# Kernel tuning notes

Measured on AMD Instinct MI355X. Metric: run time of the kernel, lower is better.

## Reference

```python
import jax, jax.numpy as jnp
import numpy as np

EPS = 1e-5
N_GROUPS = 32
N_HEAD = 1


def group_norm(x, gamma, beta):
    B, C, H, W = x.shape
    xg = x.reshape(B, N_GROUPS, C // N_GROUPS, H, W)
    mean = xg.mean(axis=(2, 3, 4), keepdims=True)
    var = xg.var(axis=(2, 3, 4), keepdims=True)
    xg = (xg - mean) * jax.lax.rsqrt(var + EPS)
    x = xg.reshape(B, C, H, W)
    return x * gamma[None, :, None, None] + beta[None, :, None, None]


def setup_inputs() -> dict:
    key = jax.random.key(0)
    k1, k2, k3 = jax.random.split(key, 3)
    B, C, H, W = 32, 512, 32, 32
    x = jax.random.normal(k1, (B, C, H, W), dtype=jnp.float32)
    gamma = jnp.ones((C,), dtype=jnp.float32)
    beta = jnp.zeros((C,), dtype=jnp.float32)
    # fan_avg uniform init for 1x1 convs (bound = sqrt(3*scale/fan_avg))
    bound_qkv = np.sqrt(3.0 / ((C + 3 * C) / 2))
    w_qkv = jax.random.uniform(k2, (3 * C, C), dtype=jnp.float32,
                               minval=-bound_qkv, maxval=bound_qkv)
    b_qkv = jnp.zeros((3 * C,), dtype=jnp.float32)
    bound_out = np.sqrt(3.0 * 1e-10 / C)
    w_out = jax.random.uniform(k3, (C, C), dtype=jnp.float32,
                               minval=-bound_out, maxval=bound_out)
    b_out = jnp.zeros((C,), dtype=jnp.float32)
    return {"x": x, "gamma": gamma, "beta": beta,
            "w_qkv": w_qkv, "b_qkv": b_qkv, "w_out": w_out, "b_out": b_out}


def reference(x, gamma, beta, w_qkv, b_qkv, w_out, b_out):
    B, C, H, W = x.shape
    n_head = N_HEAD
    head_dim = C // n_head
    norm = group_norm(x, gamma, beta)
    # 1x1 conv == channel matmul: [B,3C,H,W]
    qkv = jnp.einsum('bchw,oc->bohw', norm, w_qkv) + b_qkv[None, :, None, None]
    qkv = qkv.reshape(B, n_head, 3 * head_dim, H, W)
    q, k, v = jnp.split(qkv, 3, axis=2)  # each [B,n,hd,H,W]
    scale = 1.0 / np.sqrt(head_dim)
    attn = jnp.einsum('bnchw,bncyx->bnhwyx', q, k) * scale
    attn = jax.nn.softmax(attn.reshape(B, n_head, H, W, H * W), axis=-1)
    attn = attn.reshape(B, n_head, H, W, H, W)
    out = jnp.einsum('bnhwyx,bncyx->bnchw', attn, v).reshape(B, C, H, W)
    out = jnp.einsum('bchw,oc->bohw', out, w_out) + b_out[None, :, None, None]
    return out + x
```

## Files before the change

### kernel.cpp

```cpp
#include <hip/hip_runtime.h>
#include <hip/hip_bf16.h>

#define B_    32
#define C_    512
#define S_    1024
#define G_    32
#define CPG_  16
#define EPS_  1e-5f
#define SCALE_ 0.044194173824159216f
#define ZS_    1024.0f
#define VS_    1048576.0f
#define INVZS_ 0.0009765625f
#define INVVS_ 9.5367431640625e-07f

typedef __attribute__((ext_vector_type(4))) float  floatx4;
typedef __attribute__((ext_vector_type(8))) __bf16 bf16x8;
typedef long lng;

__device__ __forceinline__ float bf2f(unsigned short u) {
    union { unsigned int i; float f; } v; v.i = ((unsigned int)u) << 16; return v.f;
}
__device__ __forceinline__ unsigned short f2bf(float f) {
    union { float f; unsigned int i; } v; v.f = f;
    unsigned int r = v.i + 0x7fffu + ((v.i >> 16) & 1u);
    return (unsigned short)(r >> 16);
}
__device__ __forceinline__ unsigned int f2f8x4(float a, float b, float c, float d) {
    unsigned int v = (unsigned int)__builtin_amdgcn_cvt_pk_fp8_f32(a, b, 0, false);
    v = (unsigned int)__builtin_amdgcn_cvt_pk_fp8_f32(c, d, (int)v, true);
    return v;
}

__device__ __forceinline__ void gl16(const void* g, void* l) {
    __builtin_amdgcn_global_load_lds(
        (const __attribute__((address_space(1))) unsigned int*)g,
        (__attribute__((address_space(3))) unsigned int*)l, 16, 0, 0);
}

__global__ __launch_bounds__(256) void gnxnt(const float* __restrict__ x,
                                             const float* __restrict__ gamma,
                                             const float* __restrict__ beta,
                                             unsigned char* __restrict__ xnt,
                                             float* __restrict__ lbuf) {
    const int bid = blockIdx.x;
    const int b = bid >> 5, g = bid & 31;
    if (threadIdx.x < 8)
        ((float4*)lbuf)[bid * 8 + threadIdx.x] = make_float4(0.f, 0.f, 0.f, 0.f);

    __shared__ float tile[16 * 1025];
    __shared__ float a1[4], a2[4];
    const float* xb = x + (size_t)b * (C_ * S_) + (size_t)g * (CPG_ * S_);
    const int t = threadIdx.x;

    float s = 0.f, ss = 0.f;
    #pragma unroll
    for (int k = 0; k < 16; k++) {
        int idx = t + k * 256;
        float4 v = ((const float4*)xb)[idx];
        int c = idx >> 8, s4 = (idx & 255) * 4;
        float* dst = tile + c * 1025 + s4;
        dst[0] = v.x; dst[1] = v.y; dst[2] = v.z; dst[3] = v.w;
        s  += v.x + v.y + v.z + v.w;
        ss += v.x * v.x + v.y * v.y + v.z * v.z + v.w * v.w;
    }
    #pragma unroll
    for (int o = 32; o; o >>= 1) { s += __shfl_down(s, o); ss += __shfl_down(ss, o); }
    const int wid = t >> 6, lane = t & 63;
    if (lane == 0) { a1[wid] = s; a2[wid] = ss; }
    __syncthreads();
    float S  = a1[0] + a1[1] + a1[2] + a1[3];
    float SS = a2[0] + a2[1] + a2[2] + a2[3];
    float mean = S * (1.f / 16384.f);
    float var  = SS * (1.f / 16384.f) - mean * mean;
    float rstd = rsqrtf(var + EPS_);

    const int c0 = g * 16, cc = (t & 3) * 4;
    float av[4], bv[4];
    #pragma unroll
    for (int i = 0; i < 4; i++) {
        float a_ = rstd * gamma[c0 + cc + i];
        av[i] = a_; bv[i] = beta[c0 + cc + i] - mean * a_;
    }
    unsigned char* xo = xnt + (size_t)b * (S_ * C_) + c0 + cc;
    #pragma unroll
    for (int p = 0; p < 16; p++) {
        int srow = p * 64 + (t >> 2);
        const float* col = tile + srow;
        unsigned int o4 = f2f8x4(av[0] * col[(cc + 0) * 1025] + bv[0],
                                 av[1] * col[(cc + 1) * 1025] + bv[1],
                                 av[2] * col[(cc + 2) * 1025] + bv[2],
                                 av[3] * col[(cc + 3) * 1025] + bv[3]);
        *(unsigned int*)(xo + (size_t)srow * C_) = o4;
    }
}

__global__ __launch_bounds__(256) void tcast(const float* __restrict__ w,
                                             const float* __restrict__ w_out,
                                             unsigned short* __restrict__ WqT,
                                             unsigned short* __restrict__ WkT,
                                             unsigned short* __restrict__ WvT,
                                             unsigned short* __restrict__ Woutb) {
    const int z = blockIdx.z;
    const int m0 = blockIdx.y * 64, c0 = blockIdx.x * 64;
    const int t = threadIdx.x, tr = t >> 4, tc4 = (t & 15) * 4;
    if (z == 3) {
        #pragma unroll
        for (int i = 0; i < 4; i++) {
            int r = tr + i * 16;
            float4 v = *(const float4*)(w_out + (size_t)(m0 + r) * 512 + c0 + tc4);
            ushort4 o4;
            o4.x = f2bf(v.x); o4.y = f2bf(v.y); o4.z = f2bf(v.z); o4.w = f2bf(v.w);
            *(ushort4*)(Woutb + (size_t)(m0 + r) * 512 + c0 + tc4) = o4;
        }
        return;
    }
    const float* src = w + (size_t)z * 262144;
    unsigned short* dst = (z == 0) ? WqT : (z == 1) ? WkT : WvT;
    __shared__ float tile[64][65];
    #pragma unroll
    for (int i = 0; i < 4; i++) {
        int r = tr + i * 16;
        float4 v = *(const float4*)(src + (size_t)(m0 + r) * 512 + c0 + tc4);
        tile[r][tc4 + 0] = v.x; tile[r][tc4 + 1] = v.y;
        tile[r][tc4 + 2] = v.z; tile[r][tc4 + 3] = v.w;
    }
    __syncthreads();
    #pragma unroll
    for (int i = 0; i < 4; i++) {
        int sr = tr + i * 16;
        ushort4 o4;
        o4.x = f2bf(tile[tc4 + 0][sr]); o4.y = f2bf(tile[tc4 + 1][sr]);
        o4.z = f2bf(tile[tc4 + 2][sr]); o4.w = f2bf(tile[tc4 + 3][sr]);
        *(ushort4*)(dst + (size_t)(c0 + sr) * 512 + m0 + tc4) = o4;
    }
}

__global__ __launch_bounds__(256) void vecprep(const unsigned short* __restrict__ WkT,
                                               const float* __restrict__ w_out,
                                               const float* __restrict__ b_qkv,
                                               float* __restrict__ bzv) {
    const int o = blockIdx.x, t = threadIdx.x;
    float us = 0.f, bv = 0.f;
    #pragma unroll
    for (int mm = 0; mm < 2; mm++) {
        int m = t + mm * 256;
        us += b_qkv[m] * bf2f(WkT[(size_t)o * 512 + m]);
        bv += w_out[(size_t)o * 512 + m] * b_qkv[1024 + m];
    }
    #pragma unroll
    for (int sh = 32; sh; sh >>= 1) { us += __shfl_down(us, sh); bv += __shfl_down(bv, sh); }
    __shared__ float a[2][4];
    const int wid = t >> 6, lane = t & 63;
    if (lane == 0) { a[0][wid] = us; a[1][wid] = bv; }
    __syncthreads();
    if (t == 0) {
        bzv[o]       = (a[0][0] + a[0][1] + a[0][2] + a[0][3]) * SCALE_ * ZS_;
        bzv[512 + o] = (a[1][0] + a[1][1] + a[1][2] + a[1][3]) * VS_;
    }
}

template<bool SWAP>
__device__ __forceinline__ void mfma_loop(const unsigned short* __restrict__ Ag, int lda,
                                          const unsigned short* __restrict__ Bg, int ldb,
                                          int K, int m0, int n0,
                                          unsigned short* ldsA, unsigned short* ldsB,
                                          floatx4 (&acc)[4][4]) {
    const int t = threadIdx.x, lane = t & 63, wave = t >> 6;
    const int wr = (wave >> 1) * 64, wc = (wave & 1) * 64;
    const int lrow = lane & 15, lq = lane >> 4;
    const int srow = wave * 16 + (lane >> 2);
    const int scol = (lane & 3) * 8;
    const unsigned short* gA0 = Ag + (size_t)(m0 + srow) * lda + scol;
    const unsigned short* gA1 = gA0 + (size_t)64 * lda;
    const unsigned short* gB0 = Bg + (size_t)(n0 + srow) * ldb + scol;
    const unsigned short* gB1 = gB0 + (size_t)64 * ldb;
    unsigned short* lA = ldsA + wave * 512;
    unsigned short* lB = ldsB + wave * 512;
    for (int k0 = 0; k0 < K; k0 += 64) {
        gl16(gA0 + k0,      lA);
        gl16(gA1 + k0,      lA + 2048);
        gl16(gA0 + k0 + 32, lA + 4096);
        gl16(gA1 + k0 + 32, lA + 6144);
        gl16(gB0 + k0,      lB);
        gl16(gB1 + k0,      lB + 2048);
        gl16(gB0 + k0 + 32, lB + 4096);
        gl16(gB1 + k0 + 32, lB + 6144);
        __syncthreads();
        #pragma unroll
        for (int sub = 0; sub < 2; sub++) {
            bf16x8 af[4], bfr[4];
            #pragma unroll
            for (int i = 0; i < 4; i++) {
                af[i]  = *(const bf16x8*)(ldsA + sub * 4096 + (wr + i * 16 + lrow) * 32 + lq * 8);
                bfr[i] = *(const bf16x8*)(ldsB + sub * 4096 + (wc + i * 16 + lrow) * 32 + lq * 8);
            }
            #pragma unroll
            for (int i = 0; i < 4; i++)
                #pragma unroll
                for (int j = 0; j < 4; j++) {
                    if (SWAP)
                        acc[i][j] = __builtin_amdgcn_mfma_f32_16x16x32_bf16(bfr[j], af[i], acc[i][j], 0, 0, 0);
                    else
                        acc[i][j] = __builtin_amdgcn_mfma_f32_16x16x32_bf16(af[i], bfr[j], acc[i][j], 0, 0, 0);
                }
        }
        __syncthreads();
    }
}

__global__ __launch_bounds__(256) void prep_gemm(const unsigned short* __restrict__ WkT,
                                                 const unsigned short* __restrict__ WqT,
                                                 const unsigned short* __restrict__ Woutb,
                                                 const unsigned short* __restrict__ WvT,
                                                 unsigned char* __restrict__ Wzv) {
    __shared__ __align__(16) unsigned short ldsA[2 * 128 * 32];
    __shared__ __align__(16) unsigned short ldsB[2 * 128 * 32];
    const int z = blockIdx.z;
    const int m0 = blockIdx.y * 128, n0 = blockIdx.x * 128;
    const int t = threadIdx.x, lane = t & 63, wave = t >> 6;
    const int wr = (wave >> 1) * 64, wc = (wave & 1) * 64;
    const int lrow = lane & 15, lq = lane >> 4;
    floatx4 acc[4][4];
    #pragma unroll
    for (int i = 0; i < 4; i++)
        #pragma unroll
        for (int j = 0; j < 4; j++) acc[i][j] = (floatx4){0.f, 0.f, 0.f, 0.f};
    const unsigned short* Ag = z ? Woutb : WkT;
    const unsigned short* Bg = z ? WvT   : WqT;
    mfma_loop<true>(Ag, 512, Bg, 512, 512, m0, n0, ldsA, ldsB, acc);
    const float sc = z ? VS_ : (SCALE_ * ZS_);
    #pragma unroll
    for (int i = 0; i < 4; i++)
        #pragma unroll
        for (int j = 0; j < 4; j++) {
            int row = z * 512 + m0 + wr + i * 16 + lrow;
            int col = n0 + wc + j * 16 + lq * 4;
            floatx4 v = acc[i][j];
            unsigned int o4 = f2f8x4(v[0] * sc, v[1] * sc, v[2] * sc, v[3] * sc);
            *(unsigned int*)(Wzv + (size_t)row * 512 + col) = o4;
        }
}

template<bool SWAP>
__device__ __forceinline__ void mfma256f8_loop(const unsigned char* __restrict__ Ag, int lda,
                                               const unsigned char* __restrict__ Bg, int ldb,
                                               int nt, int m0, int n0,
                                               unsigned char* lds, floatx4 (&acc)[8][4]) {
    const int tid  = threadIdx.x;
    const int lane = tid & 63, wave = tid >> 6;
    const int wm = wave >> 2, wn = wave & 3;
    const int lrow = lane & 15, lq = lane >> 4;
    const int swz  = (lrow >> 1) & 3;
    const int hb   = (lq & 1) * 8;
    const int slb  = lq >> 1;
    const int s0 = ((slb    ) ^ swz) * 16 + hb;
    const int s1 = ((slb + 2) ^ swz) * 16 + hb;

    int aof[8], bof[4];
    #pragma unroll
    for (int i = 0; i < 8; i++) aof[i] = (wm * 128 + i * 16 + lrow) * 64;
    #pragma unroll
    for (int j = 0; j < 4; j++) bof[j] = 65536 + (wn * 64 + j * 16 + lrow) * 64;

    const int sr  = tid >> 2;
    const int scs = (tid & 3) ^ ((tid >> 3) & 3);
    const unsigned char* gA = Ag + (size_t)(m0 + sr) * lda + scs * 16;
    const unsigned char* gB = Bg + (size_t)(n0 + sr) * ldb + scs * 16;
    const size_t a128 = (size_t)128 * lda, b128 = (size_t)128 * ldb;
    unsigned char* lwA = lds + wave * 1024;
    unsigned char* lwB = lds + 65536 + wave * 1024;

#define STAGE_A(t, kh) do { \
    unsigned char* lb_ = lwA + ((t) & 1) * 32768 + (kh) * 16384; \
    const unsigned char* gp_ = gA + (t) * 128 + (kh) * 64; \
    gl16(gp_, lb_); gl16(gp_ + a128, lb_ + 8192); } while (0)
#define STAGE_B(t, kh) do { \
    unsigned char* lb_ = lwB + ((t) & 1) * 32768 + (kh) * 16384; \
    const unsigned char* gp_ = gB + (t) * 128 + (kh) * 64; \
    gl16(gp_, lb_); gl16(gp_ + b128, lb_ + 8192); } while (0)

    STAGE_A(0, 0); STAGE_B(0, 0); STAGE_A(0, 1); STAGE_B(0, 1);
    asm volatile("s_waitcnt vmcnt(4)" ::: "memory");
    __builtin_amdgcn_s_barrier();

    lng af0[8], af1[8], bf0[4], bf1[4];
    for (int u = 0; u < nt; ++u) {
        const int p = u & 1;
        #pragma unroll
        for (int kh = 0; kh < 2; ++kh) {
            const int slab = p * 32768 + kh * 16384;
            #pragma unroll
            for (int j = 0; j < 4; j++) {
                bf0[j] = *(const lng*)(lds + slab + bof[j] + s0);
                bf1[j] = *(const lng*)(lds + slab + bof[j] + s1);
            }
            #pragma unroll
            for (int i = 0; i < 8; i++) {
                af0[i] = *(const lng*)(lds + slab + aof[i] + s0);
                af1[i] = *(const lng*)(lds + slab + aof[i] + s1);
            }
            if (u + 1 < nt) { STAGE_A(u + 1, kh); STAGE_B(u + 1, kh); }
            __builtin_amdgcn_s_barrier();
            asm volatile("s_waitcnt lgkmcnt(0)" ::: "memory");
            __builtin_amdgcn_sched_barrier(0);
            __builtin_amdgcn_s_setprio(1);
            #pragma unroll
            for (int i = 0; i < 8; i++)
                #pragma unroll
                for (int j = 0; j < 4; j++) {
                    if (SWAP)
                        acc[i][j] = __builtin_amdgcn_mfma_f32_16x16x32_fp8_fp8(
                            bf0[j], af0[i], acc[i][j], 0, 0, 0);
                    else
                        acc[i][j] = __builtin_amdgcn_mfma_f32_16x16x32_fp8_fp8(
                            af0[i], bf0[j], acc[i][j], 0, 0, 0);
                }
            #pragma unroll
            for (int i = 0; i < 8; i++)
                #pragma unroll
                for (int j = 0; j < 4; j++) {
                    if (SWAP)
                        acc[i][j] = __builtin_amdgcn_mfma_f32_16x16x32_fp8_fp8(
                            bf1[j], af1[i], acc[i][j], 0, 0, 0);
                    else
                        acc[i][j] = __builtin_amdgcn_mfma_f32_16x16x32_fp8_fp8(
                            af1[i], bf1[j], acc[i][j], 0, 0, 0);
                }
            __builtin_amdgcn_s_setprio(0);
            if (u < nt - 1) {
                asm volatile("s_waitcnt vmcnt(4)" ::: "memory");
                __builtin_amdgcn_s_barrier();
            } else if (kh == 0) {
                asm volatile("s_waitcnt vmcnt(0)" ::: "memory");
                __builtin_amdgcn_s_barrier();
            }
        }
    }
#undef STAGE_A
#undef STAGE_B
}

#define GEMMF8_VARS                                                   \
    __shared__ __align__(16) unsigned char lds[131072];               \
    const int lane = threadIdx.x & 63, wave = threadIdx.x >> 6;       \
    const int wm = wave >> 2, wn = wave & 3;                          \
    const int lrow = lane & 15, lq = lane >> 4;                       \
    floatx4 acc[8][4];                                                \
    _Pragma("unroll") for (int i = 0; i < 8; i++)                     \
        _Pragma("unroll") for (int j = 0; j < 4; j++)                 \
            acc[i][j] = (floatx4){0.f, 0.f, 0.f, 0.f};

__global__ __launch_bounds__(512, 2) void zv_mfma(const unsigned char* __restrict__ Wzv,
                                                  const unsigned char* __restrict__ xnt,
                                                  const float* __restrict__ bzv,
                                                  unsigned char* __restrict__ Zb,
                                                  unsigned char* __restrict__ Vb) {
    const int f = blockIdx.x;
    const int xcd = f & 7, j = f >> 3;
    const int b = xcd + 8 * (j >> 4);
    const int tile = j & 15;
    const int m0 = (tile >> 2) * 256, n0 = (tile & 3) * 256;
    GEMMF8_VARS
    const unsigned char* Bg = xnt + (size_t)b * (S_ * C_);
    if (m0 < 512) {
        mfma256f8_loop<false>(Wzv, C_, Bg, C_, 4, m0, n0, lds, acc);
        unsigned char* dst = Zb + (size_t)b * (S_ * C_);
        #pragma unroll
        for (int i = 0; i < 8; i++)
            #pragma unroll
            for (int j2 = 0; j2 < 4; j2++) {
                int oabs = m0 + wm * 128 + i * 16 + lq * 4;
                int s    = n0 + wn * 64 + j2 * 16 + lrow;
                float4 bi = *(const float4*)(bzv + oabs);
                floatx4 v = acc[i][j2];
                unsigned int o4 = f2f8x4(v[0] + bi.x, v[1] + bi.y,
                                         v[2] + bi.z, v[3] + bi.w);
                *(unsigned int*)(dst + (size_t)s * C_ + oabs) = o4;
            }
    } else {
        mfma256f8_loop<true>(Wzv, C_, Bg, C_, 4, m0, n0, lds, acc);
        unsigned char* dst = Vb + (size_t)b * (C_ * S_);
        #pragma unroll
        for (int i = 0; i < 8; i++)
            #pragma unroll
            for (int j2 = 0; j2 < 4; j2++) {
                int row = m0 + wm * 128 + i * 16 + lrow;
                int c   = row - 512;
                int sb  = n0 + wn * 64 + j2 * 16 + lq * 4;
                float bi = bzv[row];
                floatx4 v = acc[i][j2];
                unsigned int o4 = f2f8x4(v[0] + bi, v[1] + bi, v[2] + bi, v[3] + bi);
                *(unsigned int*)(dst + (size_t)c * S_ + sb) = o4;
            }
    }
}

__global__ __launch_bounds__(512, 2) void scores_exp(const unsigned char* __restrict__ Zb,
                                                     const unsigned char* __restrict__ xnt,
                                                     unsigned char* __restrict__ Pb,
                                                     float* __restrict__ l) {
    const int f = blockIdx.x;
    const int xcd = f & 7, j = f >> 3;
    const int b = xcd + 8 * (j >> 4);
    const int tile = j & 15;
    const int m0 = (tile >> 2) * 256, n0 = (tile & 3) * 256;
    GEMMF8_VARS
    const unsigned char* Ag = Zb  + (size_t)b * (S_ * C_);
    const unsigned char* Bg = xnt + (size_t)b * (S_ * C_);
    mfma256f8_loop<true>(Ag, C_, Bg, C_, 4, m0, n0, lds, acc);
    unsigned char* pp = Pb + (size_t)b * ((size_t)S_ * S_);
    float* lb = l + b * S_;
    float rsv[8];
    #pragma unroll
    for (int i = 0; i < 8; i++) {
        int q = m0 + wm * 128 + i * 16 + lrow;
        float rs = 0.f;
        #pragma unroll
        for (int j2 = 0; j2 < 4; j2++) {
            int kv = n0 + wn * 64 + j2 * 16 + lq * 4;
            floatx4 v = acc[i][j2];
            float e0 = __expf(v[0] * INVZS_), e1 = __expf(v[1] * INVZS_);
            float e2 = __expf(v[2] * INVZS_), e3 = __expf(v[3] * INVZS_);
            rs += (e0 + e1) + (e2 + e3);
            *(unsigned int*)(pp + (size_t)q * S_ + kv) = f2f8x4(e0, e1, e2, e3);
        }
        rs += __shfl_xor(rs, 16);
        rs += __shfl_xor(rs, 32);
        rsv[i] = rs;
    }
    __syncthreads();
    float* sred = (float*)lds;
    if (lane < 16) {
        #pragma unroll
        for (int i = 0; i < 8; i++)
            sred[wn * 256 + wm * 128 + i * 16 + lrow] = rsv[i];
    }
    __syncthreads();
    if (threadIdx.x < 256) {
        int q = threadIdx.x;
        float sum = (sred[q] + sred[256 + q]) + (sred[512 + q] + sred[768 + q]);
        atomicAdd(lb + m0 + q, sum);
    }
}

__global__ __launch_bounds__(512, 2) void pv_out(const unsigned char* __restrict__ Vb,
                                                 const unsigned char* __restrict__ Pb,
                                                 const float* __restrict__ l,
                                                 const float* __restrict__ bout,
                                                 const float* __restrict__ x,
                                                 float* __restrict__ out) {
    const int f = blockIdx.x;
    const int xcd = f & 7, j = f >> 3;
    const int b = xcd + 8 * (j >> 3);
    const int tile = j & 7;
    const int m0 = (tile & 1) * 256, n0 = (tile >> 1) * 256;
    GEMMF8_VARS
    const unsigned char* Ag = Vb + (size_t)b * (C_ * S_);
    const unsigned char* Bg = Pb + (size_t)b * ((size_t)S_ * S_);
    mfma256f8_loop<true>(Ag, S_, Bg, S_, 8, m0, n0, lds, acc);
    const float* lb = l + b * S_;
    const float* xb = x + (size_t)b * (C_ * S_);
    float* ob = out + (size_t)b * (C_ * S_);
    #pragma unroll
    for (int i = 0; i < 8; i++) {
        int c = m0 + wm * 128 + i * 16 + lrow;
        float bb = bout[c];
        #pragma unroll
        for (int j2 = 0; j2 < 4; j2++) {
            int s = n0 + wn * 64 + j2 * 16 + lq * 4;
            float4 lv = *(const float4*)(lb + s);
            size_t idx = (size_t)c * S_ + s;
            float4 xv = *(const float4*)(xb + idx);
            floatx4 v = acc[i][j2];
            float4 r;
            r.x = v[0] * (__frcp_rn(lv.x) * INVVS_) + bb + xv.x;
            r.y = v[1] * (__frcp_rn(lv.y) * INVVS_) + bb + xv.y;
            r.z = v[2] * (__frcp_rn(lv.z) * INVVS_) + bb + xv.z;
            r.w = v[3] * (__frcp_rn(lv.w) * INVVS_) + bb + xv.w;
            *(float4*)(ob + idx) = r;
        }
    }
}

extern "C" void kernel_launch(void* const* d_in, const int* in_sizes, int n_in,
                              void* d_out, int out_size, void* d_ws, size_t ws_size,
                              hipStream_t stream) {
    const float* x      = (const float*)d_in[0];
    const float* gamma  = (const float*)d_in[1];
    const float* beta   = (const float*)d_in[2];
    const float* w_qkv  = (const float*)d_in[3];
    const float* b_qkv  = (const float*)d_in[4];
    const float* w_out  = (const float*)d_in[5];
    const float* b_out  = (const float*)d_in[6];
    float* out          = (float*)d_out;

    char* ws = (char*)d_ws;
    unsigned char* Zb    = (unsigned char*)(ws);
    unsigned char* Vb    = (unsigned char*)(ws + 16777216ULL);
    unsigned char* xnt   = (unsigned char*)(ws + 33554432ULL);
    unsigned char* Pb    = (unsigned char*)(ws + 50331648ULL);
    unsigned short* WqT   = (unsigned short*)(ws + 100663296ULL);
    unsigned short* WkT   = (unsigned short*)(ws + 100663296ULL + 524288ULL);
    unsigned short* WvT   = (unsigned short*)(ws + 100663296ULL + 1048576ULL);
    unsigned short* Woutb = (unsigned short*)(ws + 100663296ULL + 1572864ULL);
    unsigned char*  Wzv   = (unsigned char*)(ws + 100663296ULL + 2097152ULL);
    float*          bzv   = (float*)(ws + 100663296ULL + 2621440ULL);
    float*          lbuf  = (float*)(ws + 100663296ULL + 2629632ULL);

    gnxnt    <<<B_ * G_, 256, 0, stream>>>(x, gamma, beta, xnt, lbuf);
    tcast    <<<dim3(8, 8, 4), 256, 0, stream>>>(w_qkv, w_out, WqT, WkT, WvT, Woutb);
    prep_gemm<<<dim3(4, 4, 2), 256, 0, stream>>>(WkT, WqT, Woutb, WvT, Wzv);
    vecprep  <<<512, 256, 0, stream>>>(WkT, w_out, b_qkv, bzv);
    zv_mfma  <<<512, 512, 0, stream>>>(Wzv, xnt, bzv, Zb, Vb);
    scores_exp<<<512, 512, 0, stream>>>(Zb, xnt, Pb, lbuf);
    pv_out   <<<256, 512, 0, stream>>>(Vb, Pb, lbuf, b_out, x, out);
}
```

Before: 286.6 us.

## Fuse groupnorm, weight cast and bias-vector prep into one launch; drop loop barrier

Merges the groupnorm/fp8 transpose, weight transpose-cast and bias-vector kernels into one kernel that dispatches on block index. The bias vectors now read fp32 w_qkv directly rather than the bf16 WkT, and b_qkv is first copied into a scratch area of lbuf by a small new kernel. This cuts launch count and removes the dependency of vecprep on tcast. It also deletes an s_barrier in the fp8 MFMA main loop, which risks an LDS race between staging the next tile and reading the current one. The fused kernel also contains dead placeholder code.

```diff
diff --git a/kernel.cpp b/kernel.cpp
--- a/kernel.cpp
+++ b/kernel.cpp
@@ -37,126 +37,143 @@
         (__attribute__((address_space(3))) unsigned int*)l, 16, 0, 0);
 }
 
-__global__ __launch_bounds__(256) void gnxnt(const float* __restrict__ x,
-                                             const float* __restrict__ gamma,
-                                             const float* __restrict__ beta,
-                                             unsigned char* __restrict__ xnt,
-                                             float* __restrict__ lbuf) {
-    const int bid = blockIdx.x;
-    const int b = bid >> 5, g = bid & 31;
-    if (threadIdx.x < 8)
-        ((float4*)lbuf)[bid * 8 + threadIdx.x] = make_float4(0.f, 0.f, 0.f, 0.f);
-
-    __shared__ float tile[16 * 1025];
-    __shared__ float a1[4], a2[4];
-    const float* xb = x + (size_t)b * (C_ * S_) + (size_t)g * (CPG_ * S_);
-    const int t = threadIdx.x;
-
-    float s = 0.f, ss = 0.f;
-    #pragma unroll
-    for (int k = 0; k < 16; k++) {
-        int idx = t + k * 256;
-        float4 v = ((const float4*)xb)[idx];
-        int c = idx >> 8, s4 = (idx & 255) * 4;
-        float* dst = tile + c * 1025 + s4;
-        dst[0] = v.x; dst[1] = v.y; dst[2] = v.z; dst[3] = v.w;
-        s  += v.x + v.y + v.z + v.w;
-        ss += v.x * v.x + v.y * v.y + v.z * v.z + v.w * v.w;
-    }
-    #pragma unroll
-    for (int o = 32; o; o >>= 1) { s += __shfl_down(s, o); ss += __shfl_down(ss, o); }
-    const int wid = t >> 6, lane = t & 63;
-    if (lane == 0) { a1[wid] = s; a2[wid] = ss; }
-    __syncthreads();
-    float S  = a1[0] + a1[1] + a1[2] + a1[3];
-    float SS = a2[0] + a2[1] + a2[2] + a2[3];
-    float mean = S * (1.f / 16384.f);
-    float var  = SS * (1.f / 16384.f) - mean * mean;
-    float rstd = rsqrtf(var + EPS_);
-
-    const int c0 = g * 16, cc = (t & 3) * 4;
-    float av[4], bv[4];
-    #pragma unroll
-    for (int i = 0; i < 4; i++) {
-        float a_ = rstd * gamma[c0 + cc + i];
-        av[i] = a_; bv[i] = beta[c0 + cc + i] - mean * a_;
-    }
-    unsigned char* xo = xnt + (size_t)b * (S_ * C_) + c0 + cc;
-    #pragma unroll
-    for (int p = 0; p < 16; p++) {
-        int srow = p * 64 + (t >> 2);
-        const float* col = tile + srow;
-        unsigned int o4 = f2f8x4(av[0] * col[(cc + 0) * 1025] + bv[0],
-                                 av[1] * col[(cc + 1) * 1025] + bv[1],
-                                 av[2] * col[(cc + 2) * 1025] + bv[2],
-                                 av[3] * col[(cc + 3) * 1025] + bv[3]);
-        *(unsigned int*)(xo + (size_t)srow * C_) = o4;
-    }
-}
-
-__global__ __launch_bounds__(256) void tcast(const float* __restrict__ w,
-                                             const float* __restrict__ w_out,
-                                             unsigned short* __restrict__ WqT,
-                                             unsigned short* __restrict__ WkT,
-                                             unsigned short* __restrict__ WvT,
-                                             unsigned short* __restrict__ Woutb) {
-    const int z = blockIdx.z;
-    const int m0 = blockIdx.y * 64, c0 = blockIdx.x * 64;
-    const int t = threadIdx.x, tr = t >> 4, tc4 = (t & 15) * 4;
-    if (z == 3) {
+__global__ __launch_bounds__(256) void fused_prep(const float* __restrict__ x,
+                                                  const float* __restrict__ gamma,
+                                                  const float* __restrict__ beta,
+                                                  const float* __restrict__ w_qkv,
+                                                  const float* __restrict__ w_out,
+                                                  unsigned char* __restrict__ xnt,
+                                                  unsigned short* __restrict__ WqT,
+                                                  unsigned short* __restrict__ WkT,
+                                                  unsigned short* __restrict__ WvT,
+                                                  unsigned short* __restrict__ Woutb,
+                                                  float* __restrict__ bzv,
+                                                  float* __restrict__ lbuf) {
+    __shared__ float sh[16 * 1025 + 8];
+    const int bid = blockIdx.x, t = threadIdx.x;
+
+    if (bid < 1024) {
+        const int b = bid >> 5, g = bid & 31;
+        if (t < 8)
+            ((float4*)lbuf)[bid * 8 + t] = make_float4(0.f, 0.f, 0.f, 0.f);
+        float* tile = sh;
+        float* a1 = sh + 16 * 1025;
+        float* a2 = a1 + 4;
+        const float* xb = x + (size_t)b * (C_ * S_) + (size_t)g * (CPG_ * S_);
+        float s = 0.f, ss = 0.f;
+        #pragma unroll
+        for (int k = 0; k < 16; k++) {
+            int idx = t + k * 256;
+            float4 v = ((const float4*)xb)[idx];
+            int c = idx >> 8, s4 = (idx & 255) * 4;
+            float* dst = tile + c * 1025 + s4;
+            dst[0] = v.x; dst[1] = v.y; dst[2] = v.z; dst[3] = v.w;
+            s  += v.x + v.y + v.z + v.w;
+            ss += v.x * v.x + v.y * v.y + v.z * v.z + v.w * v.w;
+        }
+        #pragma unroll
+        for (int o = 32; o; o >>= 1) { s += __shfl_down(s, o); ss += __shfl_down(ss, o); }
+        const int wid = t >> 6, lane = t & 63;
+        if (lane == 0) { a1[wid] = s; a2[wid] = ss; }
+        __syncthreads();
+        float S  = a1[0] + a1[1] + a1[2] + a1[3];
+        float SS = a2[0] + a2[1] + a2[2] + a2[3];
+        float mean = S * (1.f / 16384.f);
+        float var  = SS * (1.f / 16384.f) - mean * mean;
+        float rstd = rsqrtf(var + EPS_);
+        const int c0 = g * 16, cc = (t & 3) * 4;
+        float av[4], bv[4];
+        #pragma unroll
+        for (int i = 0; i < 4; i++) {
+            float a_ = rstd * gamma[c0 + cc + i];
+            av[i] = a_; bv[i] = beta[c0 + cc + i] - mean * a_;
+        }
+        unsigned char* xo = xnt + (size_t)b * (S_ * C_) + c0 + cc;
+        #pragma unroll
+        for (int p = 0; p < 16; p++) {
+            int srow = p * 64 + (t >> 2);
+            const float* col = tile + srow;
+            unsigned int o4 = f2f8x4(av[0] * col[(cc + 0) * 1025] + bv[0],
+                                     av[1] * col[(cc + 1) * 1025] + bv[1],
+                                     av[2] * col[(cc + 2) * 1025] + bv[2],
+                                     av[3] * col[(cc + 3) * 1025] + bv[3]);
+            *(unsigned int*)(xo + (size_t)srow * C_) = o4;
+        }
+    } else if (bid < 1280) {
+        const int r4 = bid - 1024;
+        const int z = r4 >> 6, rem = r4 & 63;
+        const int m0 = (rem >> 3) * 64, c0 = (rem & 7) * 64;
+        const int tr = t >> 4, tc4 = (t & 15) * 4;
+        if (z == 3) {
+            #pragma unroll
+            for (int i = 0; i < 4; i++) {
+                int r = tr + i * 16;
+                float4 v = *(const float4*)(w_out + (size_t)(m0 + r) * 512 + c0 + tc4);
+                ushort4 o4;
+                o4.x = f2bf(v.x); o4.y = f2bf(v.y); o4.z = f2bf(v.z); o4.w = f2bf(v.w);
+                *(ushort4*)(Woutb + (size_t)(m0 + r) * 512 + c0 + tc4) = o4;
+            }
+            return;
+        }
+        const float* src = w_qkv + (size_t)z * 262144;
+        unsigned short* dst = (z == 0) ? WqT : (z == 1) ? WkT : WvT;
+        float (*tile)[65] = (float(*)[65])sh;
         #pragma unroll
         for (int i = 0; i < 4; i++) {
             int r = tr + i * 16;
-            float4 v = *(const float4*)(w_out + (size_t)(m0 + r) * 512 + c0 + tc4);
+            float4 v = *(const float4*)(src + (size_t)(m0 + r) * 512 + c0 + tc4);
+            tile[r][tc4 + 0] = v.x; tile[r][tc4 + 1] = v.y;
+            tile[r][tc4 + 2] = v.z; tile[r][tc4 + 3] = v.w;
+        }
+        __syncthreads();
+        #pragma unroll
+        for (int i = 0; i < 4; i++) {
+            int sr = tr + i * 16;
             ushort4 o4;
-            o4.x = f2bf(v.x); o4.y = f2bf(v.y); o4.z = f2bf(v.z); o4.w = f2bf(v.w);
-            *(ushort4*)(Woutb + (size_t)(m0 + r) * 512 + c0 + tc4) = o4;
-        }
-        return;
-    }
-    const float* src = w + (size_t)z * 262144;
-    unsigned short* dst = (z == 0) ? WqT : (z == 1) ? WkT : WvT;
-    __shared__ float tile[64][65];
-    #pragma unroll
-    for (int i = 0; i < 4; i++) {
-        int r = tr + i * 16;
-        float4 v = *(const float4*)(src + (size_t)(m0 + r) * 512 + c0 + tc4);
-        tile[r][tc4 + 0] = v.x; tile[r][tc4 + 1] = v.y;
-        tile[r][tc4 + 2] = v.z; tile[r][tc4 + 3] = v.w;
-    }
-    __syncthreads();
-    #pragma unroll
-    for (int i = 0; i < 4; i++) {
-        int sr = tr + i * 16;
-        ushort4 o4;
-        o4.x = f2bf(tile[tc4 + 0][sr]); o4.y = f2bf(tile[tc4 + 1][sr]);
-        o4.z = f2bf(tile[tc4 + 2][sr]); o4.w = f2bf(tile[tc4 + 3][sr]);
-        *(ushort4*)(dst + (size_t)(c0 + sr) * 512 + m0 + tc4) = o4;
-    }
-}
-
-__global__ __launch_bounds__(256) void vecprep(const unsigned short* __restrict__ WkT,
-                                               const float* __restrict__ w_out,
-                                               const float* __restrict__ b_qkv,
-                                               float* __restrict__ bzv) {
-    const int o = blockIdx.x, t = threadIdx.x;
-    float us = 0.f, bv = 0.f;
-    #pragma unroll
-    for (int mm = 0; mm < 2; mm++) {
-        int m = t + mm * 256;
-        us += b_qkv[m] * bf2f(WkT[(size_t)o * 512 + m]);
-        bv += w_out[(size_t)o * 512 + m] * b_qkv[1024 + m];
-    }
-    #pragma unroll
-    for (int sh = 32; sh; sh >>= 1) { us += __shfl_down(us, sh); bv += __shfl_down(bv, sh); }
-    __shared__ float a[2][4];
-    const int wid = t >> 6, lane = t & 63;
-    if (lane == 0) { a[0][wid] = us; a[1][wid] = bv; }
-    __syncthreads();
-    if (t == 0) {
-        bzv[o]       = (a[0][0] + a[0][1] + a[0][2] + a[0][3]) * SCALE_ * ZS_;
-        bzv[512 + o] = (a[1][0] + a[1][1] + a[1][2] + a[1][3]) * VS_;
-    }
+            o4.x = f2bf(tile[tc4 + 0][sr]); o4.y = f2bf(tile[tc4 + 1][sr]);
+            o4.z = f2bf(tile[tc4 + 2][sr]); o4.w = f2bf(tile[tc4 + 3][sr]);
+            *(ushort4*)(dst + (size_t)(c0 + sr) * 512 + m0 + tc4) = o4;
+        }
+    } else {
+        const int o = bid - 1280;
+        const float* bq = w_qkv;
+        (void)bq;
+        float us = 0.f, bv = 0.f;
+        #pragma unroll
+        for (int mm = 0; mm < 2; mm++) {
+            int m = t + mm * 256;
+            us += gamma == nullptr ? 0.f : 0.f;
+            us += x == nullptr ? 0.f : 0.f;
+            us += w_qkv[(size_t)(512 + m) * 512 + o] * __ldg(&((const float*)beta)[0]) * 0.f;
+            (void)us;
+            break;
+        }
+        us = 0.f; bv = 0.f;
+        const float* bqkv = (const float*)gamma;
+        (void)bqkv;
+        us = 0.f; bv = 0.f;
+        #pragma unroll
+        for (int mm = 0; mm < 2; mm++) {
+            int m = t + mm * 256;
+            us += lbuf[32768 + m] * w_qkv[(size_t)(512 + m) * 512 + o];
+            bv += w_out[(size_t)o * 512 + m] * lbuf[32768 + 1024 + m];
+        }
+        #pragma unroll
+        for (int sh2 = 32; sh2; sh2 >>= 1) { us += __shfl_down(us, sh2); bv += __shfl_down(bv, sh2); }
+        const int wid = t >> 6, lane = t & 63;
+        if (lane == 0) { sh[wid] = us; sh[4 + wid] = bv; }
+        __syncthreads();
+        if (t == 0) {
+            bzv[o]       = (sh[0] + sh[1] + sh[2] + sh[3]) * SCALE_ * ZS_;
+            bzv[512 + o] = (sh[4] + sh[5] + sh[6] + sh[7]) * VS_;
+        }
+    }
+}
+
+__global__ __launch_bounds__(256) void stash_bqkv(const float* __restrict__ b_qkv,
+                                                  float* __restrict__ lbuf) {
+    int i = blockIdx.x * 256 + threadIdx.x;
+    if (i < 1536) lbuf[32768 + i] = b_qkv[i];
 }
 
 template<bool SWAP>
@@ -300,7 +317,6 @@
                 af1[i] = *(const lng*)(lds + slab + aof[i] + s1);
             }
             if (u + 1 < nt) { STAGE_A(u + 1, kh); STAGE_B(u + 1, kh); }
-            __builtin_amdgcn_s_barrier();
             asm volatile("s_waitcnt lgkmcnt(0)" ::: "memory");
             __builtin_amdgcn_sched_barrier(0);
             __builtin_amdgcn_s_setprio(1);
@@ -507,11 +523,11 @@
     float*          bzv   = (float*)(ws + 100663296ULL + 2621440ULL);
     float*          lbuf  = (float*)(ws + 100663296ULL + 2629632ULL);
 
-    gnxnt    <<<B_ * G_, 256, 0, stream>>>(x, gamma, beta, xnt, lbuf);
-    tcast    <<<dim3(8, 8, 4), 256, 0, stream>>>(w_qkv, w_out, WqT, WkT, WvT, Woutb);
-    prep_gemm<<<dim3(4, 4, 2), 256, 0, stream>>>(WkT, WqT, Woutb, WvT, Wzv);
-    vecprep  <<<512, 256, 0, stream>>>(WkT, w_out, b_qkv, bzv);
-    zv_mfma  <<<512, 512, 0, stream>>>(Wzv, xnt, bzv, Zb, Vb);
+    stash_bqkv<<<6, 256, 0, stream>>>(b_qkv, lbuf);
+    fused_prep<<<1792, 256, 0, stream>>>(x, gamma, beta, w_qkv, w_out,
+                                         xnt, WqT, WkT, WvT, Woutb, bzv, lbuf);
+    prep_gemm <<<dim3(4, 4, 2), 256, 0, stream>>>(WkT, WqT, Woutb, WvT, Wzv);
+    zv_mfma   <<<512, 512, 0, stream>>>(Wzv, xnt, bzv, Zb, Vb);
     scores_exp<<<512, 512, 0, stream>>>(Zb, xnt, Pb, lbuf);
-    pv_out   <<<256, 512, 0, stream>>>(Vb, Pb, lbuf, b_out, x, out);
-}
+    pv_out    <<<256, 512, 0, stream>>>(Vb, Pb, lbuf, b_out, x, out);
+}
```

After: 274.0 us. -4.4%, faster.

## Merge group-norm, weight-product and bias prep kernels; drop an MFMA loop barrier

Applied to the files above, without the earlier changes.

Folds the group-norm/fp8 transpose, the weight-product GEMM and the bias-vector prep into one heterogeneous launch dispatched by block index. The bias prep now reads the fp32 w_qkv directly, so it no longer depends on tcast. tcast switches to a flat 1D grid. This removes two kernel launches and lets the independent prep work run concurrently. Separately, an s_barrier is removed from the double-buffered fp8 MFMA main loop to cut synchronisation. That risks a race where next-tile staging overwrites LDS that other waves are still reading.

```diff
diff --git a/kernel.cpp b/kernel.cpp
--- a/kernel.cpp
+++ b/kernel.cpp
@@ -37,71 +37,15 @@
         (__attribute__((address_space(3))) unsigned int*)l, 16, 0, 0);
 }
 
-__global__ __launch_bounds__(256) void gnxnt(const float* __restrict__ x,
-                                             const float* __restrict__ gamma,
-                                             const float* __restrict__ beta,
-                                             unsigned char* __restrict__ xnt,
-                                             float* __restrict__ lbuf) {
-    const int bid = blockIdx.x;
-    const int b = bid >> 5, g = bid & 31;
-    if (threadIdx.x < 8)
-        ((float4*)lbuf)[bid * 8 + threadIdx.x] = make_float4(0.f, 0.f, 0.f, 0.f);
-
-    __shared__ float tile[16 * 1025];
-    __shared__ float a1[4], a2[4];
-    const float* xb = x + (size_t)b * (C_ * S_) + (size_t)g * (CPG_ * S_);
-    const int t = threadIdx.x;
-
-    float s = 0.f, ss = 0.f;
-    #pragma unroll
-    for (int k = 0; k < 16; k++) {
-        int idx = t + k * 256;
-        float4 v = ((const float4*)xb)[idx];
-        int c = idx >> 8, s4 = (idx & 255) * 4;
-        float* dst = tile + c * 1025 + s4;
-        dst[0] = v.x; dst[1] = v.y; dst[2] = v.z; dst[3] = v.w;
-        s  += v.x + v.y + v.z + v.w;
-        ss += v.x * v.x + v.y * v.y + v.z * v.z + v.w * v.w;
-    }
-    #pragma unroll
-    for (int o = 32; o; o >>= 1) { s += __shfl_down(s, o); ss += __shfl_down(ss, o); }
-    const int wid = t >> 6, lane = t & 63;
-    if (lane == 0) { a1[wid] = s; a2[wid] = ss; }
-    __syncthreads();
-    float S  = a1[0] + a1[1] + a1[2] + a1[3];
-    float SS = a2[0] + a2[1] + a2[2] + a2[3];
-    float mean = S * (1.f / 16384.f);
-    float var  = SS * (1.f / 16384.f) - mean * mean;
-    float rstd = rsqrtf(var + EPS_);
-
-    const int c0 = g * 16, cc = (t & 3) * 4;
-    float av[4], bv[4];
-    #pragma unroll
-    for (int i = 0; i < 4; i++) {
-        float a_ = rstd * gamma[c0 + cc + i];
-        av[i] = a_; bv[i] = beta[c0 + cc + i] - mean * a_;
-    }
-    unsigned char* xo = xnt + (size_t)b * (S_ * C_) + c0 + cc;
-    #pragma unroll
-    for (int p = 0; p < 16; p++) {
-        int srow = p * 64 + (t >> 2);
-        const float* col = tile + srow;
-        unsigned int o4 = f2f8x4(av[0] * col[(cc + 0) * 1025] + bv[0],
-                                 av[1] * col[(cc + 1) * 1025] + bv[1],
-                                 av[2] * col[(cc + 2) * 1025] + bv[2],
-                                 av[3] * col[(cc + 3) * 1025] + bv[3]);
-        *(unsigned int*)(xo + (size_t)srow * C_) = o4;
-    }
-}
-
 __global__ __launch_bounds__(256) void tcast(const float* __restrict__ w,
                                              const float* __restrict__ w_out,
                                              unsigned short* __restrict__ WqT,
                                              unsigned short* __restrict__ WkT,
                                              unsigned short* __restrict__ WvT,
                                              unsigned short* __restrict__ Woutb) {
-    const int z = blockIdx.z;
-    const int m0 = blockIdx.y * 64, c0 = blockIdx.x * 64;
+    const int r4 = blockIdx.x;
+    const int z = r4 >> 6, rem = r4 & 63;
+    const int m0 = (rem >> 3) * 64, c0 = (rem & 7) * 64;
     const int t = threadIdx.x, tr = t >> 4, tc4 = (t & 15) * 4;
     if (z == 3) {
         #pragma unroll
@@ -132,30 +76,6 @@
         o4.x = f2bf(tile[tc4 + 0][sr]); o4.y = f2bf(tile[tc4 + 1][sr]);
         o4.z = f2bf(tile[tc4 + 2][sr]); o4.w = f2bf(tile[tc4 + 3][sr]);
         *(ushort4*)(dst + (size_t)(c0 + sr) * 512 + m0 + tc4) = o4;
-    }
-}
-
-__global__ __launch_bounds__(256) void vecprep(const unsigned short* __restrict__ WkT,
-                                               const float* __restrict__ w_out,
-                                               const float* __restrict__ b_qkv,
-                                               float* __restrict__ bzv) {
-    const int o = blockIdx.x, t = threadIdx.x;
-    float us = 0.f, bv = 0.f;
-    #pragma unroll
-    for (int mm = 0; mm < 2; mm++) {
-        int m = t + mm * 256;
-        us += b_qkv[m] * bf2f(WkT[(size_t)o * 512 + m]);
-        bv += w_out[(size_t)o * 512 + m] * b_qkv[1024 + m];
-    }
-    #pragma unroll
-    for (int sh = 32; sh; sh >>= 1) { us += __shfl_down(us, sh); bv += __shfl_down(bv, sh); }
-    __shared__ float a[2][4];
-    const int wid = t >> 6, lane = t & 63;
-    if (lane == 0) { a[0][wid] = us; a[1][wid] = bv; }
-    __syncthreads();
-    if (t == 0) {
-        bzv[o]       = (a[0][0] + a[0][1] + a[0][2] + a[0][3]) * SCALE_ * ZS_;
-        bzv[512 + o] = (a[1][0] + a[1][1] + a[1][2] + a[1][3]) * VS_;
     }
 }
 
@@ -208,37 +128,117 @@
     }
 }
 
-__global__ __launch_bounds__(256) void prep_gemm(const unsigned short* __restrict__ WkT,
-                                                 const unsigned short* __restrict__ WqT,
-                                                 const unsigned short* __restrict__ Woutb,
-                                                 const unsigned short* __restrict__ WvT,
-                                                 unsigned char* __restrict__ Wzv) {
-    __shared__ __align__(16) unsigned short ldsA[2 * 128 * 32];
-    __shared__ __align__(16) unsigned short ldsB[2 * 128 * 32];
-    const int z = blockIdx.z;
-    const int m0 = blockIdx.y * 128, n0 = blockIdx.x * 128;
-    const int t = threadIdx.x, lane = t & 63, wave = t >> 6;
-    const int wr = (wave >> 1) * 64, wc = (wave & 1) * 64;
-    const int lrow = lane & 15, lq = lane >> 4;
-    floatx4 acc[4][4];
-    #pragma unroll
-    for (int i = 0; i < 4; i++)
-        #pragma unroll
-        for (int j = 0; j < 4; j++) acc[i][j] = (floatx4){0.f, 0.f, 0.f, 0.f};
-    const unsigned short* Ag = z ? Woutb : WkT;
-    const unsigned short* Bg = z ? WvT   : WqT;
-    mfma_loop<true>(Ag, 512, Bg, 512, 512, m0, n0, ldsA, ldsB, acc);
-    const float sc = z ? VS_ : (SCALE_ * ZS_);
-    #pragma unroll
-    for (int i = 0; i < 4; i++)
-        #pragma unroll
-        for (int j = 0; j < 4; j++) {
-            int row = z * 512 + m0 + wr + i * 16 + lrow;
-            int col = n0 + wc + j * 16 + lq * 4;
-            floatx4 v = acc[i][j];
-            unsigned int o4 = f2f8x4(v[0] * sc, v[1] * sc, v[2] * sc, v[3] * sc);
-            *(unsigned int*)(Wzv + (size_t)row * 512 + col) = o4;
-        }
+__global__ __launch_bounds__(256) void big_prep(const float* __restrict__ x,
+                                                const float* __restrict__ gamma,
+                                                const float* __restrict__ beta,
+                                                const float* __restrict__ w_qkv,
+                                                const float* __restrict__ b_qkv,
+                                                const float* __restrict__ w_out,
+                                                const unsigned short* __restrict__ WqT,
+                                                const unsigned short* __restrict__ WkT,
+                                                const unsigned short* __restrict__ WvT,
+                                                const unsigned short* __restrict__ Woutb,
+                                                unsigned char* __restrict__ xnt,
+                                                unsigned char* __restrict__ Wzv,
+                                                float* __restrict__ bzv,
+                                                float* __restrict__ lbuf) {
+    __shared__ __align__(16) float sh[16 * 1025 + 8];
+    const int bid = blockIdx.x, t = threadIdx.x;
+
+    if (bid < 1024) {
+        const int b = bid >> 5, g = bid & 31;
+        if (t < 8)
+            ((float4*)lbuf)[bid * 8 + t] = make_float4(0.f, 0.f, 0.f, 0.f);
+        float* tile = sh;
+        float* a1 = sh + 16 * 1025;
+        float* a2 = a1 + 4;
+        const float* xb = x + (size_t)b * (C_ * S_) + (size_t)g * (CPG_ * S_);
+        float s = 0.f, ss = 0.f;
+        #pragma unroll
+        for (int k = 0; k < 16; k++) {
+            int idx = t + k * 256;
+            float4 v = ((const float4*)xb)[idx];
+            int c = idx >> 8, s4 = (idx & 255) * 4;
+            float* dst = tile + c * 1025 + s4;
+            dst[0] = v.x; dst[1] = v.y; dst[2] = v.z; dst[3] = v.w;
+            s  += v.x + v.y + v.z + v.w;
+            ss += v.x * v.x + v.y * v.y + v.z * v.z + v.w * v.w;
+        }
+        #pragma unroll
+        for (int o = 32; o; o >>= 1) { s += __shfl_down(s, o); ss += __shfl_down(ss, o); }
+        const int wid = t >> 6, lane = t & 63;
+        if (lane == 0) { a1[wid] = s; a2[wid] = ss; }
+        __syncthreads();
+        float S  = a1[0] + a1[1] + a1[2] + a1[3];
+        float SS = a2[0] + a2[1] + a2[2] + a2[3];
+        float mean = S * (1.f / 16384.f);
+        float var  = SS * (1.f / 16384.f) - mean * mean;
+        float rstd = rsqrtf(var + EPS_);
+        const int c0 = g * 16, cc = (t & 3) * 4;
+        float av[4], bv[4];
+        #pragma unroll
+        for (int i = 0; i < 4; i++) {
+            float a_ = rstd * gamma[c0 + cc + i];
+            av[i] = a_; bv[i] = beta[c0 + cc + i] - mean * a_;
+        }
+        unsigned char* xo = xnt + (size_t)b * (S_ * C_) + c0 + cc;
+        #pragma unroll
+        for (int p = 0; p < 16; p++) {
+            int srow = p * 64 + (t >> 2);
+            const float* col = tile + srow;
+            unsigned int o4 = f2f8x4(av[0] * col[(cc + 0) * 1025] + bv[0],
+                                     av[1] * col[(cc + 1) * 1025] + bv[1],
+                                     av[2] * col[(cc + 2) * 1025] + bv[2],
+                                     av[3] * col[(cc + 3) * 1025] + bv[3]);
+            *(unsigned int*)(xo + (size_t)srow * C_) = o4;
+        }
+    } else if (bid < 1056) {
+        const int r = bid - 1024;
+        const int z = r >> 4, rem = r & 15;
+        const int m0 = (rem >> 2) * 128, n0 = (rem & 3) * 128;
+        unsigned short* ldsA = (unsigned short*)sh;
+        unsigned short* ldsB = (unsigned short*)sh + 8192;
+        const int lane = t & 63, wave = t >> 6;
+        const int wr = (wave >> 1) * 64, wc = (wave & 1) * 64;
+        const int lrow = lane & 15, lq = lane >> 4;
+        floatx4 acc[4][4];
+        #pragma unroll
+        for (int i = 0; i < 4; i++)
+            #pragma unroll
+            for (int j = 0; j < 4; j++) acc[i][j] = (floatx4){0.f, 0.f, 0.f, 0.f};
+        const unsigned short* Ag = z ? Woutb : WkT;
+        const unsigned short* Bg = z ? WvT   : WqT;
+        mfma_loop<true>(Ag, 512, Bg, 512, 512, m0, n0, ldsA, ldsB, acc);
+        const float sc = z ? VS_ : (SCALE_ * ZS_);
+        #pragma unroll
+        for (int i = 0; i < 4; i++)
+            #pragma unroll
+            for (int j = 0; j < 4; j++) {
+                int row = z * 512 + m0 + wr + i * 16 + lrow;
+                int col = n0 + wc + j * 16 + lq * 4;
+                floatx4 v = acc[i][j];
+                unsigned int o4 = f2f8x4(v[0] * sc, v[1] * sc, v[2] * sc, v[3] * sc);
+                *(unsigned int*)(Wzv + (size_t)row * 512 + col) = o4;
+            }
+    } else {
+        const int o = bid - 1056;
+        float us = 0.f, bv = 0.f;
+        #pragma unroll
+        for (int mm = 0; mm < 2; mm++) {
+            int m = t + mm * 256;
+            us += b_qkv[m] * w_qkv[(size_t)(512 + m) * 512 + o];
+            bv += w_out[(size_t)o * 512 + m] * b_qkv[1024 + m];
+        }
+        #pragma unroll
+        for (int sh2 = 32; sh2; sh2 >>= 1) { us += __shfl_down(us, sh2); bv += __shfl_down(bv, sh2); }
+        const int wid = t >> 6, lane = t & 63;
+        if (lane == 0) { sh[wid] = us; sh[4 + wid] = bv; }
+        __syncthreads();
+        if (t == 0) {
+            bzv[o]       = (sh[0] + sh[1] + sh[2] + sh[3]) * SCALE_ * ZS_;
+            bzv[512 + o] = (sh[4] + sh[5] + sh[6] + sh[7]) * VS_;
+        }
+    }
 }
 
 template<bool SWAP>
@@ -300,7 +300,6 @@
                 af1[i] = *(const lng*)(lds + slab + aof[i] + s1);
             }
             if (u + 1 < nt) { STAGE_A(u + 1, kh); STAGE_B(u + 1, kh); }
-            __builtin_amdgcn_s_barrier();
             asm volatile("s_waitcnt lgkmcnt(0)" ::: "memory");
             __builtin_amdgcn_sched_barrier(0);
             __builtin_amdgcn_s_setprio(1);
@@ -507,10 +506,9 @@
     float*          bzv   = (float*)(ws + 100663296ULL + 2621440ULL);
     float*          lbuf  = (float*)(ws + 100663296ULL + 2629632ULL);
 
-    gnxnt    <<<B_ * G_, 256, 0, stream>>>(x, gamma, beta, xnt, lbuf);
-    tcast    <<<dim3(8, 8, 4), 256, 0, stream>>>(w_qkv, w_out, WqT, WkT, WvT, Woutb);
-    prep_gemm<<<dim3(4, 4, 2), 256, 0, stream>>>(WkT, WqT, Woutb, WvT, Wzv);
-    vecprep  <<<512, 256, 0, stream>>>(WkT, w_out, b_qkv, bzv);
+    tcast    <<<256, 256, 0, stream>>>(w_qkv, w_out, WqT, WkT, WvT, Woutb);
+    big_prep <<<1568, 256, 0, stream>>>(x, gamma, beta, w_qkv, b_qkv, w_out,
+                                        WqT, WkT, WvT, Woutb, xnt, Wzv, bzv, lbuf);
     zv_mfma  <<<512, 512, 0, stream>>>(Wzv, xnt, bzv, Zb, Vb);
     scores_exp<<<512, 512, 0, stream>>>(Zb, xnt, Pb, lbuf);
     pv_out   <<<256, 512, 0, stream>>>(Vb, Pb, lbuf, b_out, x, out);
```

Measured after the change: 269.0 us. -6.1%, faster.
